# Kernel tuning notes

Measured on AMD Instinct MI355X. Metric: run time of the kernel, lower is better.

The kernel has to match this reference:

```python
import jax, jax.numpy as jnp
import numpy as np

EPS_COS = 1e-8   # torch F.cosine_similarity norm clamp
EPS_LN = 1e-5    # torch LayerNorm eps


def setup_inputs() -> dict:
    key = jax.random.key(0)
    ks = jax.random.split(key, 8)
    B, P, T, D, H = 512, 200000, 4, 64, 256
    return {
        "target_feat": jax.random.normal(ks[0], (B, D), jnp.float32),
        "source_protos": jax.random.normal(ks[1], (P, T, D), jnp.float32),
        "W1": jax.random.normal(ks[2], (3 * D, H), jnp.float32) * 0.05,
        "b1": jnp.zeros((H,), jnp.float32),
        "ln_g": jnp.ones((H,), jnp.float32),
        "ln_b": jnp.zeros((H,), jnp.float32),
        "W2": jax.random.normal(ks[3], (H, H), jnp.float32) * 0.05,
        "b2": jnp.zeros((H,), jnp.float32),
        "W3": jax.random.normal(ks[4], (H, D), jnp.float32) * 0.05,
        "b3": jnp.zeros((D,), jnp.float32),
        "top_k": 3,
    }


def _layernorm(x, g, b):
    mu = jnp.mean(x, axis=-1, keepdims=True)
    var = jnp.mean(jnp.square(x - mu), axis=-1, keepdims=True)
    return (x - mu) * jax.lax.rsqrt(var + EPS_LN) * g + b


def reference(target_feat, source_protos, W1, b1, ln_g, ln_b, W2, b2, W3, b3, top_k):
    # --- retrieve_similar_prototypes (batched over B queries) ---
    centers = jnp.mean(source_protos, axis=1)              # [P, D]
    tn = target_feat / jnp.maximum(
        jnp.linalg.norm(target_feat, axis=-1, keepdims=True), EPS_COS)
    cn = centers / jnp.maximum(
        jnp.linalg.norm(centers, axis=-1, keepdims=True), EPS_COS)
    sims = jnp.einsum("bd,pd->bp", tn, cn)                 # [B, P] cosine sims
    top_vals, top_idx = jax.lax.top_k(sims, top_k)         # [B, K]
    similar_protos = centers[top_idx]                      # [B, K, D] gather

    # --- interpolate_new_prototype ---
    weights = jax.nn.softmax(top_vals, axis=-1)            # [B, K]
    weighted = jnp.einsum("bkd,bk->bd", similar_protos, weights)
    concat = jnp.concatenate(
        [weighted, similar_protos[:, 0], target_feat], axis=-1)  # [B, 3D]

    h = jax.nn.relu(_layernorm(concat @ W1 + b1, ln_g, ln_b))
    h = jax.nn.relu(h @ W2 + b2)
    new_proto = h @ W3 + b3                                # [B, D]
    return new_proto
```

## Files before the change

kernel.cpp:

```cpp
#include <hip/hip_runtime.h>

#define PTOT 200000
#define NB 512
#define DD 64
#define PT 256
#define NBLK ((PTOT + PT - 1) / PT)
#define NPAD (NBLK * PT)
#define NP3 (NBLK * 3)
#define NCAND 8

typedef __attribute__((ext_vector_type(4))) float f32x4;
typedef __attribute__((ext_vector_type(8))) __bf16 bf16x8;

__device__ __forceinline__ ushort f2bf(float f){
  uint u = __float_as_uint(f);
  u += 0x7FFFu + ((u >> 16) & 1u);
  return (ushort)(u >> 16);
}

__device__ __forceinline__ void ins3(uint& k0, uint& k1, uint& k2, uint key){
  uint t0 = k0 > key ? k0 : key;
  uint m0 = k0 > key ? key : k0;
  uint t1 = k1 > m0 ? k1 : m0;
  uint m1 = k1 > m0 ? m0 : k1;
  k2 = k2 > m1 ? k2 : m1;
  k1 = t1; k0 = t0;
}

__global__ __launch_bounds__(256) void kA_stream(const float* __restrict__ sp,
                                                 const float* __restrict__ tf,
                                                 ushort* __restrict__ cn,
                                                 float* __restrict__ tnf,
                                                 ushort* __restrict__ tnb){
  const int tglob = blockIdx.x * 256 + threadIdx.x;
  const int s = tglob & 15;
  const int NG = NPAD + NB;
  const int gstride = (2048 * 256) / 16;
  for (int g = tglob >> 4; g < NG; g += gstride){
    f32x4 c = {0.f, 0.f, 0.f, 0.f};
    if (g < NPAD){
      if (g < PTOT){
        const float* base = sp + (size_t)g * 256 + s * 4;
        f32x4 a0 = *(const f32x4*)(base);
        f32x4 a1 = *(const f32x4*)(base + 64);
        f32x4 a2 = *(const f32x4*)(base + 128);
        f32x4 a3 = *(const f32x4*)(base + 192);
        c = ((a0 + a1) + (a2 + a3)) * 0.25f;
      }
    } else {
      c = *(const f32x4*)(tf + (g - NPAD) * 64 + s * 4);
    }
    float ss = c.x*c.x + c.y*c.y + c.z*c.z + c.w*c.w;
    ss += __shfl_xor(ss, 1, 64);
    ss += __shfl_xor(ss, 2, 64);
    ss += __shfl_xor(ss, 4, 64);
    ss += __shfl_xor(ss, 8, 64);
    float rn = 1.0f / fmaxf(sqrtf(ss), 1e-8f);
    float n0 = c.x * rn, n1 = c.y * rn, n2 = c.z * rn, n3 = c.w * rn;
    ushort4 h;
    h.x = f2bf(n0); h.y = f2bf(n1); h.z = f2bf(n2); h.w = f2bf(n3);
    if (g < NPAD){
      *(ushort4*)(cn + (size_t)g * 64 + s * 4) = h;
    } else {
      int b = g - NPAD;
      f32x4 t = {n0, n1, n2, n3};
      *(f32x4*)(tnf + b * 64 + s * 4) = t;
      *(ushort4*)(tnb + b * 64 + s * 4) = h;
    }
  }
}

__global__ __launch_bounds__(256) void kB_scan(const ushort* __restrict__ cn,
                                               const ushort* __restrict__ tnb,
                                               uint* __restrict__ cand){
  __shared__ __align__(16) ushort lds[PT * 64];
  const int tid = threadIdx.x;
  const int blk = blockIdx.x;
  const int pbase = blk * PT;
  const int wave = tid >> 6;
  const int lane = tid & 63;
  const int l15 = lane & 15;
  const int lg  = lane >> 4;

  {
    const char* src = (const char*)(cn + (size_t)pbase * 64);
    #pragma unroll
    for (int k = 0; k < 8; ++k){
      int off = (k * 256 + tid) * 16;
      f32x4 v = *(const f32x4*)(src + off);
      int dst = off ^ (((off >> 7) & 7) << 4);
      *(f32x4*)((char*)lds + dst) = v;
    }
  }

  bf16x8 bfrag[8][2];
  #pragma unroll
  for (int bt8 = 0; bt8 < 8; ++bt8){
    int bt = wave * 8 + bt8;
    const ushort* tp = tnb + (size_t)(bt * 16 + l15) * 64 + lg * 8;
    bfrag[bt8][0] = *(const bf16x8*)(tp);
    bfrag[bt8][1] = *(const bf16x8*)(tp + 32);
  }
  __syncthreads();

  uint ka[8], kb[8], kc[8];
  #pragma unroll
  for (int i = 0; i < 8; ++i){ ka[i] = 0; kb[i] = 0; kc[i] = 0; }

  for (int ch = 0; ch < 4; ++ch){
    bf16x8 afrag[4][2];
    #pragma unroll
    for (int ps = 0; ps < 4; ++ps){
      int p = ch * 64 + ps * 16 + l15;
      #pragma unroll
      for (int kh = 0; kh < 2; ++kh){
        int byteo = (p * 128 + (kh * 32 + lg * 8) * 2) ^ ((p & 7) << 4);
        afrag[ps][kh] = *(const bf16x8*)((const char*)lds + byteo);
      }
    }
    #pragma unroll
    for (int bt8 = 0; bt8 < 8; ++bt8){
      #pragma unroll
      for (int ps = 0; ps < 4; ++ps){
        f32x4 z = {0.f, 0.f, 0.f, 0.f};
        f32x4 acc = __builtin_amdgcn_mfma_f32_16x16x32_bf16(afrag[ps][0], bfrag[bt8][0], z, 0, 0, 0);
        acc = __builtin_amdgcn_mfma_f32_16x16x32_bf16(afrag[ps][1], bfrag[bt8][1], acc, 0, 0, 0);
        #pragma unroll
        for (int j = 0; j < 4; ++j){
          int plocal = ch * 64 + ps * 16 + lg * 4 + j;
          uint key = (__float_as_uint(fmaxf(acc[j], 0.0f)) & 0xFFFFFE00u) | (uint)plocal;
          ins3(ka[bt8], kb[bt8], kc[bt8], key);
        }
      }
    }
  }
  #pragma unroll
  for (int bt8 = 0; bt8 < 8; ++bt8){
    uint a0 = ka[bt8], a1 = kb[bt8], a2 = kc[bt8];
    #pragma unroll
    for (int m = 16; m <= 32; m <<= 1){
      uint o0 = (uint)__shfl_xor((int)a0, m, 64);
      uint o1 = (uint)__shfl_xor((int)a1, m, 64);
      uint o2 = (uint)__shfl_xor((int)a2, m, 64);
      ins3(a0, a1, a2, o0); ins3(a0, a1, a2, o1); ins3(a0, a1, a2, o2);
    }
    if (lane < 16){
      int b = (wave * 8 + bt8) * 16 + l15;
      uint* dst = cand + ((size_t)blk * NB + b) * 3;
      dst[0] = a0; dst[1] = a1; dst[2] = a2;
    }
  }
}

__global__ __launch_bounds__(256) void kC_fuse(const uint* __restrict__ cand,
    const float* __restrict__ sp, const float* __restrict__ tnf,
    const float* __restrict__ tf,
    const float* __restrict__ W1, const float* __restrict__ b1,
    const float* __restrict__ lng, const float* __restrict__ lnb,
    const float* __restrict__ W2, const float* __restrict__ b2,
    const float* __restrict__ W3, const float* __restrict__ b3,
    float* __restrict__ out){
  __shared__ float cc[4][192];
  __shared__ float h1[4][256];
  __shared__ float h2[4][256];
  const int tid = threadIdx.x;
  const int lane = tid & 63;
  const int w = tid >> 6;
  const int rb = blockIdx.x * 4;
  const int b = rb + w;

  uint k0 = 0, k1 = 0, k2 = 0; int j0 = 0, j1 = 0, j2 = 0;
  for (int i = 0; i < (NP3 + 63) / 64; ++i){
    int j = lane + i * 64;
    uint k = 0;
    if (j < NP3){
      int t = j / 3, r = j - t * 3;
      k = cand[(size_t)t * (NB * 3) + b * 3 + r];
    }
    if (k > k0){ k2=k1; j2=j1; k1=k0; j1=j0; k0=k; j0=j; }
    else if (k > k1){ k2=k1; j2=j1; k1=k; j1=j; }
    else if (k > k2){ k2=k; j2=j; }
  }
  int pcand[NCAND];
  #pragma unroll
  for (int it = 0; it < NCAND; ++it){
    uint wk = k0; int wj = j0;
    #pragma unroll
    for (int m = 1; m < 64; m <<= 1){
      uint ok = (uint)__shfl_xor((int)wk, m, 64);
      int  oj = __shfl_xor(wj, m, 64);
      if (ok > wk || (ok == wk && oj > wj)){ wk = ok; wj = oj; }
    }
    pcand[it] = min((wj / 3) * PT + (int)(wk & 0x1FFu), PTOT - 1);
    if (k0 == wk && j0 == wj){ k0=k1; j0=j1; k1=k2; j1=j2; k2=0; j2=0; }
  }
  float xc[NCAND], es[NCAND];
  const float tno = tnf[b * 64 + lane];
  #pragma unroll
  for (int c = 0; c < NCAND; ++c){
    const float* base = sp + (size_t)pcand[c] * 256 + lane;
    float x = 0.25f * (base[0] + base[64] + base[128] + base[192]);
    float ss = x * x;
    float dt = x * tno;
    #pragma unroll
    for (int m = 1; m < 64; m <<= 1){
      ss += __shfl_xor(ss, m, 64);
      dt += __shfl_xor(dt, m, 64);
    }
    xc[c] = x;
    es[c] = dt / fmaxf(sqrtf(ss), 1e-8f);
  }
  float v0 = -3.0e38f, v1 = v0, v2 = v0;
  int s0 = 0, s1 = 0, s2 = 0;
  #pragma unroll
  for (int c = 0; c < NCAND; ++c){
    float v = es[c];
    if (v > v0){ v2=v1; s2=s1; v1=v0; s1=s0; v0=v; s0=c; }
    else if (v > v1){ v2=v1; s2=s1; v1=v; s1=c; }
    else if (v > v2){ v2=v; s2=c; }
  }
  float e1 = expf(v1 - v0), e2 = expf(v2 - v0);
  float inv = 1.0f / (1.0f + e1 + e2);
  float w0 = inv, w1 = e1 * inv, w2 = e2 * inv;
  float wsum = 0.f, ctop = 0.f;
  #pragma unroll
  for (int c = 0; c < NCAND; ++c){
    float coef = (c == s0) ? w0 : (c == s1) ? w1 : (c == s2) ? w2 : 0.f;
    wsum = fmaf(xc[c], coef, wsum);
    ctop += (c == s0) ? xc[c] : 0.f;
  }
  cc[w][lane]       = wsum;
  cc[w][64 + lane]  = ctop;
  cc[w][128 + lane] = tf[b * 64 + lane];
  __syncthreads();

  {
    const int h = tid;
    float a0 = b1[h]; float a1 = a0, a2 = a0, a3 = a0;
    for (int k = 0; k < 192; ++k){
      float wv = W1[k * 256 + h];
      a0 = fmaf(cc[0][k], wv, a0);
      a1 = fmaf(cc[1][k], wv, a1);
      a2 = fmaf(cc[2][k], wv, a2);
      a3 = fmaf(cc[3][k], wv, a3);
    }
    h1[0][h] = a0; h1[1][h] = a1; h1[2][h] = a2; h1[3][h] = a3;
  }
  __syncthreads();
  {
    float v[4]; float s = 0.f, q = 0.f;
    #pragma unroll
    for (int j = 0; j < 4; ++j){
      v[j] = h1[w][lane + 64 * j];
      s += v[j]; q += v[j] * v[j];
    }
    #pragma unroll
    for (int m = 1; m < 64; m <<= 1){
      s += __shfl_xor(s, m, 64);
      q += __shfl_xor(q, m, 64);
    }
    float mu = s * (1.0f / 256.0f);
    float var = q * (1.0f / 256.0f) - mu * mu;
    float rs = rsqrtf(var + 1e-5f);
    #pragma unroll
    for (int j = 0; j < 4; ++j){
      int hh = lane + 64 * j;
      float y = (v[j] - mu) * rs * lng[hh] + lnb[hh];
      h1[w][hh] = fmaxf(y, 0.0f);
    }
  }
  __syncthreads();
  {
    const int h = tid;
    float a0 = b2[h]; float a1 = a0, a2 = a0, a3 = a0;
    for (int k = 0; k < 256; ++k){
      float wv = W2[k * 256 + h];
      a0 = fmaf(h1[0][k], wv, a0);
      a1 = fmaf(h1[1][k], wv, a1);
      a2 = fmaf(h1[2][k], wv, a2);
      a3 = fmaf(h1[3][k], wv, a3);
    }
    h2[0][h] = fmaxf(a0, 0.f); h2[1][h] = fmaxf(a1, 0.f);
    h2[2][h] = fmaxf(a2, 0.f); h2[3][h] = fmaxf(a3, 0.f);
  }
  __syncthreads();
  {
    const int d = tid & 63, q = tid >> 6;
    float a = b3[d];
    for (int k = 0; k < 256; ++k)
      a = fmaf(h2[q][k], W3[k * 64 + d], a);
    out[(size_t)(rb + q) * 64 + d] = a;
  }
}

extern "C" void kernel_launch(void* const* d_in, const int* in_sizes, int n_in,
                              void* d_out, int out_size, void* d_ws, size_t ws_size,
                              hipStream_t stream){
  const float* tf = (const float*)d_in[0];
  const float* sp = (const float*)d_in[1];
  const float* W1 = (const float*)d_in[2];
  const float* b1 = (const float*)d_in[3];
  const float* lng = (const float*)d_in[4];
  const float* lnb = (const float*)d_in[5];
  const float* W2 = (const float*)d_in[6];
  const float* b2 = (const float*)d_in[7];
  const float* W3 = (const float*)d_in[8];
  const float* b3 = (const float*)d_in[9];
  float* out = (float*)d_out;

  char* ws = (char*)d_ws;
  const size_t off_tnb  = 0;
  const size_t off_tnf  = 65536;
  const size_t off_cn   = 65536 + 131072;
  const size_t cn_bytes = (size_t)NPAD * 64 * 2;
  const size_t off_cand = off_cn + cn_bytes;
  const size_t need = off_cand + (size_t)NBLK * NB * 3 * 4;
  if (ws_size < need) return;

  ushort* tnb = (ushort*)(ws + off_tnb);
  float*  tnf = (float*)(ws + off_tnf);
  ushort* cnb = (ushort*)(ws + off_cn);
  uint*   cand = (uint*)(ws + off_cand);

  kA_stream<<<2048, 256, 0, stream>>>(sp, tf, cnb, tnf, tnb);
  kB_scan<<<NBLK, 256, 0, stream>>>(cnb, tnb, cand);
  kC_fuse<<<NB / 4, 256, 0, stream>>>(cand, sp, tnf, tf,
                                      W1, b1, lng, lnb, W2, b2, W3, b3, out);
}
```

Measured before the change: 131.4 us.

## Restructure scan kernel loops to cut register pressure and raise occupancy

The scan kernel's loop nest is inverted so each wave processes one query tile at a time across all 256 prototypes. It keeps only one set of B fragments and one top-3 state in registers, instead of 8 fragment pairs and 24 key registers. Launch bounds now request 4 blocks per CU. The intent is to cut VGPR usage so more waves can hide LDS and MFMA latency. In exchange, every query tile re-reads the A fragments from LDS, multiplying LDS traffic by 8, and the top-k insertion chain becomes serially dependent per tile.

```diff
diff --git a/kernel.cpp b/kernel.cpp
--- a/kernel.cpp
+++ b/kernel.cpp
@@ -70,20 +70,19 @@
   }
 }
 
-__global__ __launch_bounds__(256) void kB_scan(const ushort* __restrict__ cn,
-                                               const ushort* __restrict__ tnb,
-                                               uint* __restrict__ cand){
+__global__ __launch_bounds__(256, 4) void kB_scan(const ushort* __restrict__ cn,
+                                                  const ushort* __restrict__ tnb,
+                                                  uint* __restrict__ cand){
   __shared__ __align__(16) ushort lds[PT * 64];
   const int tid = threadIdx.x;
   const int blk = blockIdx.x;
-  const int pbase = blk * PT;
   const int wave = tid >> 6;
   const int lane = tid & 63;
   const int l15 = lane & 15;
   const int lg  = lane >> 4;
 
   {
-    const char* src = (const char*)(cn + (size_t)pbase * 64);
+    const char* src = (const char*)(cn + (size_t)blk * PT * 64);
     #pragma unroll
     for (int k = 0; k < 8; ++k){
       int off = (k * 256 + tid) * 16;
@@ -92,62 +91,43 @@
       *(f32x4*)((char*)lds + dst) = v;
     }
   }
-
-  bf16x8 bfrag[8][2];
-  #pragma unroll
+  __syncthreads();
+
+  #pragma unroll 2
   for (int bt8 = 0; bt8 < 8; ++bt8){
-    int bt = wave * 8 + bt8;
+    const int bt = wave * 8 + bt8;
     const ushort* tp = tnb + (size_t)(bt * 16 + l15) * 64 + lg * 8;
-    bfrag[bt8][0] = *(const bf16x8*)(tp);
-    bfrag[bt8][1] = *(const bf16x8*)(tp + 32);
-  }
-  __syncthreads();
-
-  uint ka[8], kb[8], kc[8];
-  #pragma unroll
-  for (int i = 0; i < 8; ++i){ ka[i] = 0; kb[i] = 0; kc[i] = 0; }
-
-  for (int ch = 0; ch < 4; ++ch){
-    bf16x8 afrag[4][2];
-    #pragma unroll
-    for (int ps = 0; ps < 4; ++ps){
-      int p = ch * 64 + ps * 16 + l15;
+    bf16x8 bf0 = *(const bf16x8*)(tp);
+    bf16x8 bf1 = *(const bf16x8*)(tp + 32);
+    uint k0 = 0, k1 = 0, k2 = 0;
+    #pragma unroll 4
+    for (int ps = 0; ps < 16; ++ps){
+      const int p = ps * 16 + l15;
+      const int base = p * 128;
+      const int sw = (p & 7) << 4;
+      bf16x8 a0 = *(const bf16x8*)((const char*)lds + ((base + lg * 16) ^ sw));
+      bf16x8 a1 = *(const bf16x8*)((const char*)lds + ((base + 64 + lg * 16) ^ sw));
+      f32x4 z = {0.f, 0.f, 0.f, 0.f};
+      f32x4 acc = __builtin_amdgcn_mfma_f32_16x16x32_bf16(a0, bf0, z, 0, 0, 0);
+      acc = __builtin_amdgcn_mfma_f32_16x16x32_bf16(a1, bf1, acc, 0, 0, 0);
       #pragma unroll
-      for (int kh = 0; kh < 2; ++kh){
-        int byteo = (p * 128 + (kh * 32 + lg * 8) * 2) ^ ((p & 7) << 4);
-        afrag[ps][kh] = *(const bf16x8*)((const char*)lds + byteo);
+      for (int j = 0; j < 4; ++j){
+        uint key = (__float_as_uint(fmaxf(acc[j], 0.0f)) & 0xFFFFFE00u)
+                 | (uint)(ps * 16 + lg * 4 + j);
+        ins3(k0, k1, k2, key);
       }
     }
     #pragma unroll
-    for (int bt8 = 0; bt8 < 8; ++bt8){
-      #pragma unroll
-      for (int ps = 0; ps < 4; ++ps){
-        f32x4 z = {0.f, 0.f, 0.f, 0.f};
-        f32x4 acc = __builtin_amdgcn_mfma_f32_16x16x32_bf16(afrag[ps][0], bfrag[bt8][0], z, 0, 0, 0);
-        acc = __builtin_amdgcn_mfma_f32_16x16x32_bf16(afrag[ps][1], bfrag[bt8][1], acc, 0, 0, 0);
-        #pragma unroll
-        for (int j = 0; j < 4; ++j){
-          int plocal = ch * 64 + ps * 16 + lg * 4 + j;
-          uint key = (__float_as_uint(fmaxf(acc[j], 0.0f)) & 0xFFFFFE00u) | (uint)plocal;
-          ins3(ka[bt8], kb[bt8], kc[bt8], key);
-        }
-      }
-    }
-  }
-  #pragma unroll
-  for (int bt8 = 0; bt8 < 8; ++bt8){
-    uint a0 = ka[bt8], a1 = kb[bt8], a2 = kc[bt8];
-    #pragma unroll
     for (int m = 16; m <= 32; m <<= 1){
-      uint o0 = (uint)__shfl_xor((int)a0, m, 64);
-      uint o1 = (uint)__shfl_xor((int)a1, m, 64);
-      uint o2 = (uint)__shfl_xor((int)a2, m, 64);
-      ins3(a0, a1, a2, o0); ins3(a0, a1, a2, o1); ins3(a0, a1, a2, o2);
+      uint o0 = (uint)__shfl_xor((int)k0, m, 64);
+      uint o1 = (uint)__shfl_xor((int)k1, m, 64);
+      uint o2 = (uint)__shfl_xor((int)k2, m, 64);
+      ins3(k0, k1, k2, o0); ins3(k0, k1, k2, o1); ins3(k0, k1, k2, o2);
     }
     if (lane < 16){
-      int b = (wave * 8 + bt8) * 16 + l15;
+      int b = bt * 16 + l15;
       uint* dst = cand + ((size_t)blk * NB + b) * 3;
-      dst[0] = a0; dst[1] = a1; dst[2] = a2;
+      dst[0] = k0; dst[1] = k1; dst[2] = k2;
     }
   }
 }
```

Result: slower. 134.4 us (+2.3%).
